# Kernel tuning notes

Hardware: AMD Instinct MI355X
Metric: run time of the kernel (lower is better)

Reference implementation:

```python
import jax, jax.numpy as jnp
import numpy as np

H = 16          # head_num
DH = 64         # h_size = all_head_size // head_num
HIDDEN = 1024
ALL_HEAD = 1024
B, S = 4, 2048
NEG = -1000000000.0


def setup_inputs() -> dict:
    key = jax.random.key(0)
    ks = jax.random.split(key, 8)
    x = jax.random.normal(ks[0], (B, S, HIDDEN), dtype=jnp.float32)
    y = jax.random.normal(ks[1], (B, S, HIDDEN), dtype=jnp.float32)
    attention_mask = jax.random.randint(ks[2], (B, 1, S, S), 0, 2, dtype=jnp.int32)
    sc = 1.0 / np.sqrt(HIDDEN)
    Wq = jax.random.normal(ks[3], (HIDDEN, ALL_HEAD), dtype=jnp.float32) * sc
    Wk = jax.random.normal(ks[4], (HIDDEN, ALL_HEAD), dtype=jnp.float32) * sc
    Wv = jax.random.normal(ks[5], (HIDDEN, ALL_HEAD), dtype=jnp.float32) * sc
    Wo = jax.random.normal(ks[6], (ALL_HEAD, HIDDEN), dtype=jnp.float32) * (1.0 / np.sqrt(ALL_HEAD))
    bo = jnp.zeros((HIDDEN,), dtype=jnp.float32)
    return {"x": x, "y": y, "Wq": Wq, "Wk": Wk, "Wv": Wv, "Wo": Wo, "bo": bo,
            "attention_mask": attention_mask}


def reference(x, y, Wq, Wk, Wv, Wo, bo, attention_mask):
    b = x.shape[0]
    # projections, split heads: [B, H, S, Dh]
    q = (x @ Wq).reshape(b, -1, H, DH).transpose(0, 2, 1, 3)
    k = (x @ Wk).reshape(b, -1, H, DH).transpose(0, 2, 1, 3)
    v = (y @ Wv).reshape(b, -1, H, DH).transpose(0, 2, 1, 3)
    mask = attention_mask == 0  # True => masked (matches .eq(0))
    scores = jnp.einsum('bhqd,bhkd->bhqk', q, k)
    scores = jnp.where(mask, NEG, scores)  # masked_fill BEFORE scaling, as in source
    attn = jax.nn.softmax(scores / np.sqrt(DH), axis=-1)
    ctx = jnp.einsum('bhqk,bhkd->bhqd', attn, v)
    ctx = ctx.transpose(0, 2, 1, 3).reshape(b, -1, H * DH)
    return ctx @ Wo + bo  # dropout p=0.0 is identity
```

## Files before the change

kernel.cpp:

```cpp
#include <hip/hip_runtime.h>
#include <hip/hip_bf16.h>
#include <stdint.h>

typedef __attribute__((ext_vector_type(8))) short short8;
typedef __attribute__((ext_vector_type(4))) float f32x4;
typedef __attribute__((ext_vector_type(16))) float f32x16;
typedef __hip_bfloat16 bf16;

typedef __attribute__((address_space(3))) uint32_t lds_u32_t;
typedef __attribute__((address_space(1))) const uint32_t glb_u32_t;

__device__ __forceinline__ void gload_lds16(const void* g, void* l) {
  __builtin_amdgcn_global_load_lds((glb_u32_t*)g, (lds_u32_t*)l, 16, 0, 0);
}

__device__ __forceinline__ uint32_t cvt_pk_bf16(float lo, float hi_) {
  uint32_t r;
  asm volatile("v_cvt_pk_bf16_f32 %0, %1, %2" : "=v"(r) : "v"(lo), "v"(hi_));
  return r;
}

__device__ __forceinline__ void plane32swap(uint32_t &a, uint32_t &b) {
  auto r = __builtin_amdgcn_permlane32_swap((int)a, (int)b, false, false);
  a = (uint32_t)r[0]; b = (uint32_t)r[1];
}


__global__ void conv_bf16(const float* __restrict__ in, bf16* __restrict__ outp, int n4) {
  int i = blockIdx.x * blockDim.x + threadIdx.x;
  if (i >= n4) return;
  const float4 v = ((const float4*)in)[i];
  union { ushort4 u; bf16 h[4]; } o;
  o.h[0] = __float2bfloat16(v.x); o.h[1] = __float2bfloat16(v.y);
  o.h[2] = __float2bfloat16(v.z); o.h[3] = __float2bfloat16(v.w);
  ((ushort4*)outp)[i] = o.u;
}

__global__ void transpose_w(const float* __restrict__ W0, const float* __restrict__ W1,
                            const float* __restrict__ W2, const float* __restrict__ W3,
                            bf16* __restrict__ outp) {
  const float* W = blockIdx.z == 0 ? W0 : blockIdx.z == 1 ? W1 : blockIdx.z == 2 ? W2 : W3;
  bf16* o = outp + (size_t)blockIdx.z * 1048576;
  __shared__ float t[32][33];
  int x = threadIdx.x, y0 = threadIdx.y;
  int c0 = blockIdx.x * 32, r0 = blockIdx.y * 32;
#pragma unroll
  for (int i = 0; i < 4; i++)
    t[y0 + i*8][x] = W[(size_t)(r0 + y0 + i*8)*1024 + c0 + x];
  __syncthreads();
#pragma unroll
  for (int i = 0; i < 4; i++)
    o[(size_t)(c0 + y0 + i*8)*1024 + r0 + x] = __float2bfloat16(t[x][y0 + i*8]);
}

__global__ void maskpack(const int* __restrict__ mask, unsigned long long* __restrict__ mbits) {
  int tid = threadIdx.x;
  int lane = tid & 63, wid = tid >> 6;
  size_t word = (size_t)blockIdx.x * 4 + wid;
  int v = mask[word * 64 + lane];
  unsigned long long bits = __ballot(v == 0);
  if (lane == 0) mbits[word] = bits;
}

template<int MODE>
__global__ void gemm_bt(const bf16* __restrict__ A, const bf16* __restrict__ Bt,
                        void* __restrict__ Out, const float* __restrict__ bias) {
  const int tid = threadIdx.x;
  const int lane = tid & 63, wid = tid >> 6;
  const int g = lane >> 4, c = lane & 15;
  const int m0 = blockIdx.x * 128, n0 = blockIdx.y * 128;
  const int wm = wid >> 1, wn = wid & 1;
  __shared__ bf16 As[128 * 64];
  __shared__ bf16 Bs[128 * 64];
  f32x4 acc[4][4] = {};
  for (int k0 = 0; k0 < 1024; k0 += 64) {
#pragma unroll
    for (int i = 0; i < 4; i++) {
      int chunk = wid * 4 + i;
      int idx = chunk * 64 + lane;
      int row = idx >> 3, u = idx & 7;
      int koff = k0 + ((u ^ (row & 7)) * 8);
      gload_lds16(A  + (size_t)(m0 + row) * 1024 + koff, As + chunk * 512);
      gload_lds16(Bt + (size_t)(n0 + row) * 1024 + koff, Bs + chunk * 512);
    }
    __syncthreads();
#pragma unroll
    for (int kk = 0; kk < 2; kk++) {
      short8 af[4], bf_[4];
#pragma unroll
      for (int f = 0; f < 4; f++) {
        int ra = wm * 64 + f * 16 + c;
        af[f]  = *(const short8*)(As + ra * 64 + (((kk * 4 + g) ^ (ra & 7)) * 8));
        int rb = wn * 64 + f * 16 + c;
        bf_[f] = *(const short8*)(Bs + rb * 64 + (((kk * 4 + g) ^ (rb & 7)) * 8));
      }
#pragma unroll
      for (int fm = 0; fm < 4; fm++)
#pragma unroll
        for (int fn = 0; fn < 4; fn++)
          acc[fm][fn] = __builtin_amdgcn_mfma_f32_16x16x32_bf16(af[fm], bf_[fn], acc[fm][fn], 0, 0, 0);
    }
    __syncthreads();
  }
#pragma unroll
  for (int fm = 0; fm < 4; fm++) {
#pragma unroll
    for (int fn = 0; fn < 4; fn++) {
      int gn = n0 + wn * 64 + fn * 16 + c;
#pragma unroll
      for (int r = 0; r < 4; r++) {
        int gm = m0 + wm * 64 + fm * 16 + g * 4 + r;
        float v = acc[fm][fn][r];
        if constexpr (MODE == 2) {
          ((float*)Out)[(size_t)gm * 1024 + gn] = v + bias[gn];
        } else if constexpr (MODE == 0) {
          int b = gm >> 11, s = gm & 2047, hh = gn >> 6, d = gn & 63;
          ((bf16*)Out)[(((size_t)b * 16 + hh) * 2048 + s) * 64 + d] = __float2bfloat16(v);
        } else {
          int b = gm >> 11, s = gm & 2047, hh = gn >> 6, d = gn & 63;
          ((bf16*)Out)[(((size_t)b * 16 + hh) * 64 + d) * 2048 + s] = __float2bfloat16(v);
        }
      }
    }
  }
}

__global__ __launch_bounds__(256, 4) void attn_kernel(
    const bf16* __restrict__ Qb, const bf16* __restrict__ Kb, const bf16* __restrict__ Vt,
    const unsigned long long* __restrict__ mbits, bf16* __restrict__ ctx) {
  const int tid = threadIdx.x;
  const int lane = tid & 63, wid = tid >> 6;
  const int c5 = lane & 31, hi = lane >> 5;
  const int sid = blockIdx.x;
  const int xcd = sid & 7, idx = sid >> 3;
  const int bh = xcd * 8 + (idx >> 4);
  const int qb0 = (idx & 15) * 128 + wid * 32;
  const int b = bh >> 4, h = bh & 15;
  __shared__ bf16 Ks[2][64 * 64];
  __shared__ bf16 Vs[2][64 * 64];
  const bf16* Qp = Qb + (size_t)bh * 2048 * 64;
  const bf16* Kp = Kb + (size_t)bh * 2048 * 64;
  const bf16* Vp = Vt + (size_t)bh * 64 * 2048;
  const unsigned long long* mrow = mbits + ((size_t)b * 2048 + qb0 + c5) * 32;

  auto stage = [&](int kt, int sel) {
#pragma unroll
    for (int i = 0; i < 2; i++) {
      int chunk = wid * 2 + i;
      int idx2 = chunk * 64 + lane;
      int row = idx2 >> 3, u = idx2 & 7;
      gload_lds16(Kp + (size_t)(kt * 64 + row) * 64 + ((u ^ (row & 7)) * 8), &Ks[sel][chunk * 512]);
      gload_lds16(Vp + (size_t)row * 2048 + kt * 64 + ((u ^ (row & 7)) * 8), &Vs[sel][chunk * 512]);
    }
  };

  short8 qf[4];
#pragma unroll
  for (int ks = 0; ks < 4; ks++)
    qf[ks] = *(const short8*)(Qp + (size_t)(qb0 + c5) * 64 + ks * 16 + hi * 8);

  f32x16 Oacc0 = {}, Oacc1 = {};
  float mrun = -3.0e38f, mc1 = 0.f, lrun = 0.f;

  const float C1 = 0.18033688011112042f;
  const float THRRAW = 44.36f;

  unsigned long long mwC, mwN;
  stage(0, 0);
  mwC = mrow[0];
  __syncthreads();

#pragma unroll 2
  for (int kt = 0; kt < 32; kt++) {
    const int sel = kt & 1;
    if (kt < 31) stage(kt + 1, sel ^ 1);
    mwN = mrow[(kt + 1) & 31];

    f32x16 s0 = {}, s1 = {};
    __builtin_amdgcn_s_setprio(1);
#pragma unroll
    for (int ks = 0; ks < 4; ks++) {
      short8 aK0 = *(const short8*)(&Ks[sel][(c5)      * 64 + (((ks * 2 + hi) ^ (c5 & 7)) * 8)]);
      short8 aK1 = *(const short8*)(&Ks[sel][(32 + c5) * 64 + (((ks * 2 + hi) ^ (c5 & 7)) * 8)]);
      s0 = __builtin_amdgcn_mfma_f32_32x32x16_bf16(aK0, qf[ks], s0, 0, 0, 0);
      s1 = __builtin_amdgcn_mfma_f32_32x32x16_bf16(aK1, qf[ks], s1, 0, 0, 0);
    }
    __builtin_amdgcn_s_setprio(0);
    float lmx = fmaxf(s0[0], s1[0]);
#pragma unroll
    for (int reg = 1; reg < 16; reg++)
      lmx = fmaxf(fmaxf(s0[reg], s1[reg]), lmx);
    if (__any(lmx > mrun + THRRAW)) {
      float rmx = fmaxf(lmx, __shfl_xor(lmx, 32));
      float mnew = fmaxf(mrun, rmx);
      float sc = exp2f((mrun - mnew) * C1);
      mrun = mnew; mc1 = mnew * C1;
      lrun *= sc;
#pragma unroll
      for (int reg = 0; reg < 16; reg++) {
        const int qrow = (reg & 3) + 8 * (reg >> 2) + 4 * hi;
        float srow = __shfl(sc, qrow);
        Oacc0[reg] *= srow; Oacc1[reg] *= srow;
      }
    }
    const uint32_t nlo = ~(((uint32_t)mwC)         >> (4 * hi));
    const uint32_t nhi = ~(((uint32_t)(mwC >> 32)) >> (4 * hi));
    uint32_t pk0[8], pk1[8];
    float lsum = 0.f;
#pragma unroll
    for (int r8 = 0; r8 < 8; r8++) {
      const int rA = 2 * r8, rB = 2 * r8 + 1;
      const int pA = (rA & 3) + 8 * (rA >> 2), pB = (rB & 3) + 8 * (rB >> 2);
      float a0 = exp2f(fmaf(s0[rA], C1, -mc1));
      float a1 = exp2f(fmaf(s0[rB], C1, -mc1));
      float b0 = exp2f(fmaf(s1[rA], C1, -mc1));
      float b1 = exp2f(fmaf(s1[rB], C1, -mc1));
      a0 = __uint_as_float(__float_as_uint(a0) & (uint32_t)(((int32_t)(nlo << (31 - pA))) >> 31));
      a1 = __uint_as_float(__float_as_uint(a1) & (uint32_t)(((int32_t)(nlo << (31 - pB))) >> 31));
      b0 = __uint_as_float(__float_as_uint(b0) & (uint32_t)(((int32_t)(nhi << (31 - pA))) >> 31));
      b1 = __uint_as_float(__float_as_uint(b1) & (uint32_t)(((int32_t)(nhi << (31 - pB))) >> 31));
      lsum += (a0 + a1) + (b0 + b1);
      pk0[r8] = cvt_pk_bf16(a0, a1);
      pk1[r8] = cvt_pk_bf16(b0, b1);
    }
    lrun += lsum;
    short8 pa[4];
#pragma unroll
    for (int ks = 0; ks < 4; ks++) {
      const int e0 = 2 * ((2 * ks) & 3);
      const int e1 = 2 * ((2 * ks + 1) & 3);
      uint32_t w0, w1, w2, w3;
      if (ks < 2) { w0 = pk0[e0];     w2 = pk0[e1];
                    w1 = pk0[e0 + 1]; w3 = pk0[e1 + 1]; }
      else        { w0 = pk1[e0];     w2 = pk1[e1];
                    w1 = pk1[e0 + 1]; w3 = pk1[e1 + 1]; }
      plane32swap(w0, w2);
      plane32swap(w1, w3);
      union { uint32_t u[4]; short8 s; } pu;
      pu.u[0] = w0; pu.u[1] = w1; pu.u[2] = w2; pu.u[3] = w3;
      pa[ks] = pu.s;
    }
    __builtin_amdgcn_s_setprio(1);
#pragma unroll
    for (int ks = 0; ks < 4; ks++) {
      short8 bV0 = *(const short8*)(&Vs[sel][(c5)      * 64 + (((ks * 2 + hi) ^ (c5 & 7)) * 8)]);
      short8 bV1 = *(const short8*)(&Vs[sel][(32 + c5) * 64 + (((ks * 2 + hi) ^ (c5 & 7)) * 8)]);
      Oacc0 = __builtin_amdgcn_mfma_f32_32x32x16_bf16(pa[ks], bV0, Oacc0, 0, 0, 0);
      Oacc1 = __builtin_amdgcn_mfma_f32_32x32x16_bf16(pa[ks], bV1, Oacc1, 0, 0, 0);
    }
    __builtin_amdgcn_s_setprio(0);
    mwC = mwN;
    __syncthreads();
  }
  float lfull = lrun + __shfl_xor(lrun, 32);
#pragma unroll
  for (int reg = 0; reg < 16; reg++) {
    const int qrow = (reg & 3) + 8 * (reg >> 2) + 4 * hi;
    float linv = __builtin_amdgcn_rcpf(__shfl(lfull, qrow));
    size_t base = ((size_t)b * 2048 + qb0 + qrow) * 1024 + h * 64;
    ctx[base + c5]      = __float2bfloat16(Oacc0[reg] * linv);
    ctx[base + 32 + c5] = __float2bfloat16(Oacc1[reg] * linv);
  }
}


extern "C" void kernel_launch(void* const* d_in, const int* in_sizes, int n_in,
                              void* d_out, int out_size, void* d_ws, size_t ws_size,
                              hipStream_t stream) {
  const float* x  = (const float*)d_in[0];
  const float* y  = (const float*)d_in[1];
  const float* Wq = (const float*)d_in[2];
  const float* Wk = (const float*)d_in[3];
  const float* Wv = (const float*)d_in[4];
  const float* Wo = (const float*)d_in[5];
  const float* bo = (const float*)d_in[6];
  const int* amask = (const int*)d_in[7];
  float* out = (float*)d_out;

  char* ws = (char*)d_ws;
  bf16* xb = (bf16*)ws;
  bf16* yb = (bf16*)(ws + 16777216);
  bf16* WT = (bf16*)(ws + 33554432);
  bf16* Qb = (bf16*)(ws + 41943040);
  bf16* Kb = (bf16*)(ws + 58720256);
  bf16* Vt = (bf16*)(ws + 75497472);
  unsigned long long* mbits = (unsigned long long*)(ws + 92274688);
  bf16* ctx = xb;

  conv_bf16<<<8192, 256, 0, stream>>>(x, xb, 2097152);
  conv_bf16<<<8192, 256, 0, stream>>>(y, yb, 2097152);
  transpose_w<<<dim3(32, 32, 4), dim3(32, 8), 0, stream>>>(Wq, Wk, Wv, Wo, WT);
  maskpack<<<65536, 256, 0, stream>>>(amask, mbits);

  dim3 gg(64, 8);
  gemm_bt<0><<<gg, 256, 0, stream>>>(xb, WT + 0 * 1048576, Qb, nullptr);
  gemm_bt<0><<<gg, 256, 0, stream>>>(xb, WT + 1 * 1048576, Kb, nullptr);
  gemm_bt<1><<<gg, 256, 0, stream>>>(yb, WT + 2 * 1048576, Vt, nullptr);

  attn_kernel<<<1024, 256, 0, stream>>>(Qb, Kb, Vt, mbits, ctx);

  gemm_bt<2><<<gg, 256, 0, stream>>>(ctx, WT + 3 * 1048576, out, bo);
}
```

Measured before the change: 301.2 us.

## Pipeline PV matmul with next QK in attention and merge projection GEMMs

The attention loop now defers each tile's P·V MFMA to the next iteration, issuing it right after the next tile's QK MFMAs. This lets matrix work overlap the softmax exponent and mask VALU work. K/V LDS buffers go from double to triple buffering to keep the deferred V tile resident, and the occupancy hint drops from 4 to 3 blocks per CU. Separately, the Q, K and V projection GEMMs are fused into a single launch over a wider grid, which cuts launch count and improves wave fill. The costs are more registers held live (paP) and more LDS per block.

```diff
diff --git a/kernel.cpp b/kernel.cpp
--- a/kernel.cpp
+++ b/kernel.cpp
@@ -62,9 +62,71 @@
   if (lane == 0) mbits[word] = bits;
 }
 
-template<int MODE>
-__global__ void gemm_bt(const bf16* __restrict__ A, const bf16* __restrict__ Bt,
-                        void* __restrict__ Out, const float* __restrict__ bias) {
+__global__ void gemm_proj(const bf16* __restrict__ xb, const bf16* __restrict__ yb,
+                          const bf16* __restrict__ Bt, bf16* __restrict__ Qb,
+                          bf16* __restrict__ Kb, bf16* __restrict__ Vt) {
+  const int tid = threadIdx.x;
+  const int lane = tid & 63, wid = tid >> 6;
+  const int g = lane >> 4, c = lane & 15;
+  const int m0 = blockIdx.x * 128, n0 = blockIdx.y * 128;
+  const int wm = wid >> 1, wn = wid & 1;
+  const bf16* A = (blockIdx.y < 16) ? xb : yb;
+  __shared__ bf16 As[128 * 64];
+  __shared__ bf16 Bs[128 * 64];
+  f32x4 acc[4][4] = {};
+  for (int k0 = 0; k0 < 1024; k0 += 64) {
+#pragma unroll
+    for (int i = 0; i < 4; i++) {
+      int chunk = wid * 4 + i;
+      int idx = chunk * 64 + lane;
+      int row = idx >> 3, u = idx & 7;
+      int koff = k0 + ((u ^ (row & 7)) * 8);
+      gload_lds16(A  + (size_t)(m0 + row) * 1024 + koff, As + chunk * 512);
+      gload_lds16(Bt + (size_t)(n0 + row) * 1024 + koff, Bs + chunk * 512);
+    }
+    __syncthreads();
+#pragma unroll
+    for (int kk = 0; kk < 2; kk++) {
+      short8 af[4], bf_[4];
+#pragma unroll
+      for (int f = 0; f < 4; f++) {
+        int ra = wm * 64 + f * 16 + c;
+        af[f]  = *(const short8*)(As + ra * 64 + (((kk * 4 + g) ^ (ra & 7)) * 8));
+        int rb = wn * 64 + f * 16 + c;
+        bf_[f] = *(const short8*)(Bs + rb * 64 + (((kk * 4 + g) ^ (rb & 7)) * 8));
+      }
+#pragma unroll
+      for (int fm = 0; fm < 4; fm++)
+#pragma unroll
+        for (int fn = 0; fn < 4; fn++)
+          acc[fm][fn] = __builtin_amdgcn_mfma_f32_16x16x32_bf16(af[fm], bf_[fn], acc[fm][fn], 0, 0, 0);
+    }
+    __syncthreads();
+  }
+#pragma unroll
+  for (int fm = 0; fm < 4; fm++) {
+#pragma unroll
+    for (int fn = 0; fn < 4; fn++) {
+      int gn = n0 + wn * 64 + fn * 16 + c;
+      int gnl = gn & 1023, hh = gnl >> 6, d = gnl & 63;
+#pragma unroll
+      for (int r = 0; r < 4; r++) {
+        int gm = m0 + wm * 64 + fm * 16 + g * 4 + r;
+        int b = gm >> 11, s = gm & 2047;
+        float v = acc[fm][fn][r];
+        if (blockIdx.y < 16) {
+          bf16* O = (blockIdx.y < 8) ? Qb : Kb;
+          O[(((size_t)b * 16 + hh) * 2048 + s) * 64 + d] = __float2bfloat16(v);
+        } else {
+          Vt[(((size_t)b * 16 + hh) * 64 + d) * 2048 + s] = __float2bfloat16(v);
+        }
+      }
+    }
+  }
+}
+
+__global__ void gemm_bt2(const bf16* __restrict__ A, const bf16* __restrict__ Bt,
+                         float* __restrict__ Out, const float* __restrict__ bias) {
   const int tid = threadIdx.x;
   const int lane = tid & 63, wid = tid >> 6;
   const int g = lane >> 4, c = lane & 15;
@@ -103,29 +165,19 @@
     __syncthreads();
   }
 #pragma unroll
-  for (int fm = 0; fm < 4; fm++) {
+  for (int fm = 0; fm < 4; fm++)
 #pragma unroll
     for (int fn = 0; fn < 4; fn++) {
       int gn = n0 + wn * 64 + fn * 16 + c;
 #pragma unroll
       for (int r = 0; r < 4; r++) {
         int gm = m0 + wm * 64 + fm * 16 + g * 4 + r;
-        float v = acc[fm][fn][r];
-        if constexpr (MODE == 2) {
-          ((float*)Out)[(size_t)gm * 1024 + gn] = v + bias[gn];
-        } else if constexpr (MODE == 0) {
-          int b = gm >> 11, s = gm & 2047, hh = gn >> 6, d = gn & 63;
-          ((bf16*)Out)[(((size_t)b * 16 + hh) * 2048 + s) * 64 + d] = __float2bfloat16(v);
-        } else {
-          int b = gm >> 11, s = gm & 2047, hh = gn >> 6, d = gn & 63;
-          ((bf16*)Out)[(((size_t)b * 16 + hh) * 64 + d) * 2048 + s] = __float2bfloat16(v);
-        }
-      }
-    }
-  }
-}
-
-__global__ __launch_bounds__(256, 4) void attn_kernel(
+        Out[(size_t)gm * 1024 + gn] = acc[fm][fn][r] + bias[gn];
+      }
+    }
+}
+
+__global__ __launch_bounds__(256, 3) void attn_kernel(
     const bf16* __restrict__ Qb, const bf16* __restrict__ Kb, const bf16* __restrict__ Vt,
     const unsigned long long* __restrict__ mbits, bf16* __restrict__ ctx) {
   const int tid = threadIdx.x;
@@ -136,21 +188,21 @@
   const int bh = xcd * 8 + (idx >> 4);
   const int qb0 = (idx & 15) * 128 + wid * 32;
   const int b = bh >> 4, h = bh & 15;
-  __shared__ bf16 Ks[2][64 * 64];
-  __shared__ bf16 Vs[2][64 * 64];
+  __shared__ bf16 Ks[3][64 * 64];
+  __shared__ bf16 Vs[3][64 * 64];
   const bf16* Qp = Qb + (size_t)bh * 2048 * 64;
   const bf16* Kp = Kb + (size_t)bh * 2048 * 64;
   const bf16* Vp = Vt + (size_t)bh * 64 * 2048;
   const unsigned long long* mrow = mbits + ((size_t)b * 2048 + qb0 + c5) * 32;
 
-  auto stage = [&](int kt, int sel) {
+  auto stage = [&](int kt, int s3) {
 #pragma unroll
     for (int i = 0; i < 2; i++) {
       int chunk = wid * 2 + i;
       int idx2 = chunk * 64 + lane;
       int row = idx2 >> 3, u = idx2 & 7;
-      gload_lds16(Kp + (size_t)(kt * 64 + row) * 64 + ((u ^ (row & 7)) * 8), &Ks[sel][chunk * 512]);
-      gload_lds16(Vp + (size_t)row * 2048 + kt * 64 + ((u ^ (row & 7)) * 8), &Vs[sel][chunk * 512]);
+      gload_lds16(Kp + (size_t)(kt * 64 + row) * 64 + ((u ^ (row & 7)) * 8), &Ks[s3][chunk * 512]);
+      gload_lds16(Vp + (size_t)row * 2048 + kt * 64 + ((u ^ (row & 7)) * 8), &Vs[s3][chunk * 512]);
     }
   };
 
@@ -161,6 +213,7 @@
 
   f32x16 Oacc0 = {}, Oacc1 = {};
   float mrun = -3.0e38f, mc1 = 0.f, lrun = 0.f;
+  short8 paP[4];
 
   const float C1 = 0.18033688011112042f;
   const float THRRAW = 44.36f;
@@ -170,10 +223,10 @@
   mwC = mrow[0];
   __syncthreads();
 
-#pragma unroll 2
+  int sel = 0, selp = 2;
   for (int kt = 0; kt < 32; kt++) {
-    const int sel = kt & 1;
-    if (kt < 31) stage(kt + 1, sel ^ 1);
+    const int seln = (sel == 2) ? 0 : sel + 1;
+    if (kt < 31) stage(kt + 1, seln);
     mwN = mrow[(kt + 1) & 31];
 
     f32x16 s0 = {}, s1 = {};
@@ -184,6 +237,15 @@
       short8 aK1 = *(const short8*)(&Ks[sel][(32 + c5) * 64 + (((ks * 2 + hi) ^ (c5 & 7)) * 8)]);
       s0 = __builtin_amdgcn_mfma_f32_32x32x16_bf16(aK0, qf[ks], s0, 0, 0, 0);
       s1 = __builtin_amdgcn_mfma_f32_32x32x16_bf16(aK1, qf[ks], s1, 0, 0, 0);
+    }
+    if (kt > 0) {
+#pragma unroll
+      for (int ks = 0; ks < 4; ks++) {
+        short8 bV0 = *(const short8*)(&Vs[selp][(c5)      * 64 + (((ks * 2 + hi) ^ (c5 & 7)) * 8)]);
+        short8 bV1 = *(const short8*)(&Vs[selp][(32 + c5) * 64 + (((ks * 2 + hi) ^ (c5 & 7)) * 8)]);
+        Oacc0 = __builtin_amdgcn_mfma_f32_32x32x16_bf16(paP[ks], bV0, Oacc0, 0, 0, 0);
+        Oacc1 = __builtin_amdgcn_mfma_f32_32x32x16_bf16(paP[ks], bV1, Oacc1, 0, 0, 0);
+      }
     }
     __builtin_amdgcn_s_setprio(0);
     float lmx = fmaxf(s0[0], s1[0]);
@@ -224,7 +286,6 @@
       pk1[r8] = cvt_pk_bf16(b0, b1);
     }
     lrun += lsum;
-    short8 pa[4];
 #pragma unroll
     for (int ks = 0; ks < 4; ks++) {
       const int e0 = 2 * ((2 * ks) & 3);
@@ -238,19 +299,18 @@
       plane32swap(w1, w3);
       union { uint32_t u[4]; short8 s; } pu;
       pu.u[0] = w0; pu.u[1] = w1; pu.u[2] = w2; pu.u[3] = w3;
-      pa[ks] = pu.s;
-    }
-    __builtin_amdgcn_s_setprio(1);
-#pragma unroll
-    for (int ks = 0; ks < 4; ks++) {
-      short8 bV0 = *(const short8*)(&Vs[sel][(c5)      * 64 + (((ks * 2 + hi) ^ (c5 & 7)) * 8)]);
-      short8 bV1 = *(const short8*)(&Vs[sel][(32 + c5) * 64 + (((ks * 2 + hi) ^ (c5 & 7)) * 8)]);
-      Oacc0 = __builtin_amdgcn_mfma_f32_32x32x16_bf16(pa[ks], bV0, Oacc0, 0, 0, 0);
-      Oacc1 = __builtin_amdgcn_mfma_f32_32x32x16_bf16(pa[ks], bV1, Oacc1, 0, 0, 0);
-    }
-    __builtin_amdgcn_s_setprio(0);
+      paP[ks] = pu.s;
+    }
     mwC = mwN;
-    __syncthreads();
+    selp = sel; sel = seln;
+    __syncthreads();
+  }
+#pragma unroll
+  for (int ks = 0; ks < 4; ks++) {
+    short8 bV0 = *(const short8*)(&Vs[selp][(c5)      * 64 + (((ks * 2 + hi) ^ (c5 & 7)) * 8)]);
+    short8 bV1 = *(const short8*)(&Vs[selp][(32 + c5) * 64 + (((ks * 2 + hi) ^ (c5 & 7)) * 8)]);
+    Oacc0 = __builtin_amdgcn_mfma_f32_32x32x16_bf16(paP[ks], bV0, Oacc0, 0, 0, 0);
+    Oacc1 = __builtin_amdgcn_mfma_f32_32x32x16_bf16(paP[ks], bV1, Oacc1, 0, 0, 0);
   }
   float lfull = lrun + __shfl_xor(lrun, 32);
 #pragma unroll
@@ -292,12 +352,9 @@
   transpose_w<<<dim3(32, 32, 4), dim3(32, 8), 0, stream>>>(Wq, Wk, Wv, Wo, WT);
   maskpack<<<65536, 256, 0, stream>>>(amask, mbits);
 
-  dim3 gg(64, 8);
-  gemm_bt<0><<<gg, 256, 0, stream>>>(xb, WT + 0 * 1048576, Qb, nullptr);
-  gemm_bt<0><<<gg, 256, 0, stream>>>(xb, WT + 1 * 1048576, Kb, nullptr);
-  gemm_bt<1><<<gg, 256, 0, stream>>>(yb, WT + 2 * 1048576, Vt, nullptr);
+  gemm_proj<<<dim3(64, 24), 256, 0, stream>>>(xb, yb, WT, Qb, Kb, Vt);
 
   attn_kernel<<<1024, 256, 0, stream>>>(Qb, Kb, Vt, mbits, ctx);
 
-  gemm_bt<2><<<gg, 256, 0, stream>>>(ctx, WT + 3 * 1048576, out, bo);
-}
+  gemm_bt2<<<dim3(64, 8), 256, 0, stream>>>(ctx, WT + 3 * 1048576, out, bo);
+}
```

New measurement: 302.5 us. Within noise of the previous version (+0.4%).
